# Kernel optimization log

Measured on AMD Instinct MI355X. Metric: run time of the kernel, lower is better.

The kernel has to match this reference:

```python
import jax, jax.numpy as jnp
import numpy as np

DIM = 512
HEADS = 8
HEAD_DIM = DIM // HEADS
MLP_HIDDEN = int(DIM * 4.0)
B, N = 4, 2048
LS_INIT = 1e-5
EPS = 1e-5


def _layernorm(x, w, b):
    mu = jnp.mean(x, axis=-1, keepdims=True)
    var = jnp.mean(jnp.square(x - mu), axis=-1, keepdims=True)
    return (x - mu) * jax.lax.rsqrt(var + EPS) * w + b


def setup_inputs() -> dict:
    key = jax.random.key(0)
    ks = jax.random.split(key, 12)
    s = 0.02
    return {
        "x": jax.random.normal(ks[0], (B, N, DIM), jnp.float32),
        "rel_pos_bias": jax.random.normal(ks[1], (HEADS, N, N), jnp.float32),
        "qkv_w": jax.random.normal(ks[2], (DIM, 3 * DIM), jnp.float32) * s,
        "qkv_b": jnp.zeros((3 * DIM,), jnp.float32),
        "out_w": jax.random.normal(ks[3], (DIM, DIM), jnp.float32) * s,
        "out_b": jnp.zeros((DIM,), jnp.float32),
        "ln1_w": jnp.ones((DIM,), jnp.float32),
        "ln1_b": jnp.zeros((DIM,), jnp.float32),
        "ln2_w": jnp.ones((DIM,), jnp.float32),
        "ln2_b": jnp.zeros((DIM,), jnp.float32),
        "ffn_w1": jax.random.normal(ks[4], (DIM, MLP_HIDDEN), jnp.float32) * s,
        "ffn_b1": jnp.zeros((MLP_HIDDEN,), jnp.float32),
        "ffn_w2": jax.random.normal(ks[5], (MLP_HIDDEN, DIM), jnp.float32) * s,
        "ffn_b2": jnp.zeros((DIM,), jnp.float32),
        "gamma1": jnp.full((DIM,), LS_INIT, jnp.float32),
        "gamma2": jnp.full((DIM,), LS_INIT, jnp.float32),
    }


def reference(x, rel_pos_bias, qkv_w, qkv_b, out_w, out_b, ln1_w, ln1_b,
              ln2_w, ln2_b, ffn_w1, ffn_b1, ffn_w2, ffn_b2, gamma1, gamma2):
    # Pre-norm MHA with relative-position bias
    y = _layernorm(x, ln1_w, ln1_b)                       # [B,N,C]
    qkv = y @ qkv_w + qkv_b                               # [B,N,3C]
    qkv = qkv.reshape(B, N, 3, HEADS, HEAD_DIM)
    q = jnp.transpose(qkv[:, :, 0], (0, 2, 1, 3))         # [B,H,N,D]
    k = jnp.transpose(qkv[:, :, 1], (0, 2, 1, 3))
    v = jnp.transpose(qkv[:, :, 2], (0, 2, 1, 3))
    scale = 1.0 / np.sqrt(HEAD_DIM).astype(np.float32)
    attn = jnp.einsum("bhid,bhjd->bhij", q, k) * scale    # [B,H,N,N]
    attn = attn + rel_pos_bias[None]
    attn = jax.nn.softmax(attn, axis=-1)
    out = jnp.einsum("bhij,bhjd->bhid", attn, v)          # [B,H,N,D]
    out = jnp.transpose(out, (0, 2, 1, 3)).reshape(B, N, DIM)
    out = out @ out_w + out_b
    x = x + out * gamma1                                  # layer scale, no drop-path (eval)
    # FFN with exact GELU
    y2 = _layernorm(x, ln2_w, ln2_b)
    h = jax.nn.gelu(y2 @ ffn_w1 + ffn_b1, approximate=False)
    ffn_out = h @ ffn_w2 + ffn_b2
    x = x + ffn_out * gamma2
    return x
```

## Files before the change

### kernel.cpp

```cpp
#include <hip/hip_runtime.h>
#include <hip/hip_bf16.h>
#include <math.h>

#define SEQ 2048
#define BATCH 4
#define DM 512
#define NH 8
#define HD 64
#define HID 2048
#define ROWS (BATCH * SEQ)

typedef __attribute__((ext_vector_type(8))) short short8;
typedef __attribute__((ext_vector_type(4))) float f32x4;

__device__ __forceinline__ short f2bf(float f) {
    unsigned u = __float_as_uint(f);
    u += 0x7fff + ((u >> 16) & 1);
    return (short)(u >> 16);
}

__device__ __forceinline__ void gl2lds16(const void* g, void* l) {
    __builtin_amdgcn_global_load_lds(
        (const __attribute__((address_space(1))) void*)g,
        (__attribute__((address_space(3))) void*)l, 16, 0, 0);
}

__global__ __launch_bounds__(256) void tcast_all(
    const float* __restrict__ qkv_w, const float* __restrict__ out_w,
    const float* __restrict__ w1, const float* __restrict__ w2,
    short* __restrict__ o_qkv, short* __restrict__ o_out,
    short* __restrict__ o_w1, short* __restrict__ o_w2) {
    __shared__ float tile[32][33];
    int id = blockIdx.x;
    const float* W; short* O; int K, N;
    if (id < 768)       { W = qkv_w; O = o_qkv; K = 512;  N = 1536; }
    else if (id < 1024) { W = out_w; O = o_out; K = 512;  N = 512;  id -= 768; }
    else if (id < 2048) { W = w1;    O = o_w1;  K = 512;  N = 2048; id -= 1024; }
    else                { W = w2;    O = o_w2;  K = 2048; N = 512;  id -= 2048; }
    int tn = N / 32;
    int n0 = (id % tn) * 32, k0 = (id / tn) * 32;
    int tx = threadIdx.x, ty = threadIdx.y;
#pragma unroll
    for (int i = 0; i < 4; ++i)
        tile[ty + i * 8][tx] = W[(size_t)(k0 + ty + i * 8) * N + n0 + tx];
    __syncthreads();
#pragma unroll
    for (int i = 0; i < 4; ++i)
        O[(size_t)(n0 + ty + i * 8) * K + k0 + tx] = f2bf(tile[tx][ty + i * 8]);
}

__global__ __launch_bounds__(256) void bias_prep(const float* __restrict__ bias,
                                                 short* __restrict__ biasP) {
    __shared__ float tl[4][16][68];
    int t = threadIdx.x;
    int w = t >> 6, ln = t & 63;
    int quad = ln >> 4, l15 = ln & 15;
    int tau = blockIdx.x * 4 + w;
    int jtK = tau & 31;
    int g = (tau >> 5) & 127;
    int h = tau >> 12;
    const float* src = bias + (size_t)h * SEQ * SEQ + (size_t)g * 16 * SEQ + jtK * 64;
#pragma unroll
    for (int i = 0; i < 4; ++i) {
        int row = i * 4 + quad;
        int col = l15 * 4;
        *(float4*)&tl[w][row][col] = *(const float4*)(src + (size_t)row * SEQ + col);
    }
    short* dst = biasP + (size_t)tau * 1024 + ln * 4;
#pragma unroll
    for (int ni = 0; ni < 4; ++ni) {
        float4 v = *(const float4*)&tl[w][l15][ni * 16 + quad * 4];
        float2 lo, hi;
        lo.x = v.x * 1.44269504f; lo.y = v.y * 1.44269504f;
        hi.x = v.z * 1.44269504f; hi.y = v.w * 1.44269504f;
        __hip_bfloat162 l2 = __float22bfloat162_rn(lo);
        __hip_bfloat162 h2 = __float22bfloat162_rn(hi);
        uint2 pp;
        pp.x = *(unsigned*)&l2;
        pp.y = *(unsigned*)&h2;
        *(uint2*)(dst + (size_t)ni * 256) = pp;
    }
}

__global__ __launch_bounds__(256) void ln_k(const float* __restrict__ X,
                                            const float* __restrict__ g,
                                            const float* __restrict__ bta,
                                            short* __restrict__ Y) {
    int t = threadIdx.x;
    int wv = t >> 6, ln = t & 63;
    size_t row = (size_t)blockIdx.x * 4 + wv;
    const float* xr = X + row * DM;
    float4 v0 = *(const float4*)(xr + ln * 4);
    float4 v1 = *(const float4*)(xr + 256 + ln * 4);
    float s = v0.x + v0.y + v0.z + v0.w + v1.x + v1.y + v1.z + v1.w;
    float q = v0.x * v0.x + v0.y * v0.y + v0.z * v0.z + v0.w * v0.w +
              v1.x * v1.x + v1.y * v1.y + v1.z * v1.z + v1.w * v1.w;
#pragma unroll
    for (int off = 1; off < 64; off <<= 1) {
        s += __shfl_xor(s, off);
        q += __shfl_xor(q, off);
    }
    float mean = s * (1.0f / 512.0f);
    float var = q * (1.0f / 512.0f) - mean * mean;
    float rstd = rsqrtf(var + 1e-5f);
    int c0 = ln * 4, c1 = 256 + ln * 4;
    ushort4 o0, o1;
    o0.x = (unsigned short)f2bf((v0.x - mean) * rstd * g[c0 + 0] + bta[c0 + 0]);
    o0.y = (unsigned short)f2bf((v0.y - mean) * rstd * g[c0 + 1] + bta[c0 + 1]);
    o0.z = (unsigned short)f2bf((v0.z - mean) * rstd * g[c0 + 2] + bta[c0 + 2]);
    o0.w = (unsigned short)f2bf((v0.w - mean) * rstd * g[c0 + 3] + bta[c0 + 3]);
    o1.x = (unsigned short)f2bf((v1.x - mean) * rstd * g[c1 + 0] + bta[c1 + 0]);
    o1.y = (unsigned short)f2bf((v1.y - mean) * rstd * g[c1 + 1] + bta[c1 + 1]);
    o1.z = (unsigned short)f2bf((v1.z - mean) * rstd * g[c1 + 2] + bta[c1 + 2]);
    o1.w = (unsigned short)f2bf((v1.w - mean) * rstd * g[c1 + 3] + bta[c1 + 3]);
    *(ushort4*)((unsigned short*)Y + row * DM + c0) = o0;
    *(ushort4*)((unsigned short*)Y + row * DM + c1) = o1;
}

template <int EPI, int TN>
__global__ __launch_bounds__(256) void gemm_bt(const short* __restrict__ A,
                                               const short* __restrict__ Bt,
                                               const float* __restrict__ bias,
                                               const float* __restrict__ gamma,
                                               const float* __restrict__ res,
                                               void* __restrict__ Cout,
                                               short* __restrict__ Cout2,
                                               int M, int N, int K) {
    constexpr int NI = TN / 32;
    __shared__ __attribute__((aligned(16))) short As0[128][32];
    __shared__ __attribute__((aligned(16))) short As1[128][32];
    __shared__ __attribute__((aligned(16))) short Bs0[TN][32];
    __shared__ __attribute__((aligned(16))) short Bs1[TN][32];
    int t = threadIdx.x;
    int w = t >> 6, ln = t & 63;
    int quad = ln >> 4, l15 = ln & 15;
    int n0 = blockIdx.x * TN, m0 = blockIdx.y * 128;
    int wm = (w & 1) * 64, wn = (w >> 1) * (TN / 2);

    int srow0 = w * 32 + (ln >> 2);
    int srow1 = srow0 + 16;
    int srowB = w * 16 + (ln >> 2);
    int schunk = (ln & 3) * 8;
    const short* Ag0 = A + (size_t)(m0 + srow0) * K + schunk;
    const short* Ag1 = A + (size_t)(m0 + srow1) * K + schunk;
    const short* Bg0 = Bt + (size_t)(n0 + srow0) * K + schunk;
    const short* Bg1 = Bt + (size_t)(n0 + srow1) * K + schunk;
    const short* BgB = Bt + (size_t)(n0 + srowB) * K + schunk;

    f32x4 acc[4][NI];
#pragma unroll
    for (int i = 0; i < 4; ++i)
#pragma unroll
        for (int j = 0; j < NI; ++j) acc[i][j] = (f32x4){0.f, 0.f, 0.f, 0.f};

    for (int k0 = 0; k0 < K; k0 += 64) {
        __syncthreads();
        gl2lds16(Ag0 + k0, &As0[srow0][schunk]);
        gl2lds16(Ag1 + k0, &As0[srow1][schunk]);
        gl2lds16(Ag0 + k0 + 32, &As1[srow0][schunk]);
        gl2lds16(Ag1 + k0 + 32, &As1[srow1][schunk]);
        if (TN == 128) {
            gl2lds16(Bg0 + k0, &Bs0[srow0 & (TN - 1)][schunk]);
            gl2lds16(Bg1 + k0, &Bs0[srow1 & (TN - 1)][schunk]);
            gl2lds16(Bg0 + k0 + 32, &Bs1[srow0 & (TN - 1)][schunk]);
            gl2lds16(Bg1 + k0 + 32, &Bs1[srow1 & (TN - 1)][schunk]);
        } else {
            gl2lds16(BgB + k0, &Bs0[srowB & (TN - 1)][schunk]);
            gl2lds16(BgB + k0 + 32, &Bs1[srowB & (TN - 1)][schunk]);
        }
        __syncthreads();
        {
            short8 af[4], bf[NI];
#pragma unroll
            for (int mi = 0; mi < 4; ++mi)
                af[mi] = *(const short8*)&As0[wm + mi * 16 + l15][quad * 8];
#pragma unroll
            for (int ni = 0; ni < NI; ++ni)
                bf[ni] = *(const short8*)&Bs0[wn + ni * 16 + l15][quad * 8];
#pragma unroll
            for (int mi = 0; mi < 4; ++mi)
#pragma unroll
                for (int ni = 0; ni < NI; ++ni)
                    acc[mi][ni] = __builtin_amdgcn_mfma_f32_16x16x32_bf16(
                        af[mi], bf[ni], acc[mi][ni], 0, 0, 0);
        }
        {
            short8 af[4], bf[NI];
#pragma unroll
            for (int mi = 0; mi < 4; ++mi)
                af[mi] = *(const short8*)&As1[wm + mi * 16 + l15][quad * 8];
#pragma unroll
            for (int ni = 0; ni < NI; ++ni)
                bf[ni] = *(const short8*)&Bs1[wn + ni * 16 + l15][quad * 8];
#pragma unroll
            for (int mi = 0; mi < 4; ++mi)
#pragma unroll
                for (int ni = 0; ni < NI; ++ni)
                    acc[mi][ni] = __builtin_amdgcn_mfma_f32_16x16x32_bf16(
                        af[mi], bf[ni], acc[mi][ni], 0, 0, 0);
        }
    }

    if (EPI == 3 && n0 >= 1024) {
#pragma unroll
        for (int mi = 0; mi < 4; ++mi) {
#pragma unroll
            for (int ni = 0; ni < NI; ++ni) {
                int col = n0 + wn + ni * 16 + l15;
                int d = col - 1024, hh = d >> 6, dd = d & 63;
                int row0 = m0 + wm + mi * 16 + quad * 4;
                int bb = row0 >> 11, key = row0 & 2047;
                float bs = bias[col];
                ushort4 pk;
                pk.x = (unsigned short)f2bf(acc[mi][ni][0] + bs);
                pk.y = (unsigned short)f2bf(acc[mi][ni][1] + bs);
                pk.z = (unsigned short)f2bf(acc[mi][ni][2] + bs);
                pk.w = (unsigned short)f2bf(acc[mi][ni][3] + bs);
                *(ushort4*)&Cout2[((size_t)(bb * 8 + hh) * 64 + dd) * 2048 + key] = pk;
            }
        }
    } else {
#pragma unroll
        for (int mi = 0; mi < 4; ++mi) {
#pragma unroll
            for (int ni = 0; ni < NI; ++ni) {
#pragma unroll
                for (int r = 0; r < 4; ++r) {
                    int row = m0 + wm + mi * 16 + quad * 4 + r;
                    int col = n0 + wn + ni * 16 + l15;
                    float v = acc[mi][ni][r] + bias[col];
                    if (EPI == 0) {
                        ((short*)Cout)[(size_t)row * N + col] = f2bf(v);
                    } else if (EPI == 1) {
                        float u = v * fmaf(v * v, 0.0713548162f, 1.59576912f);
                        float gg = v / (1.0f + __expf(-u));
                        ((short*)Cout)[(size_t)row * N + col] = f2bf(gg);
                    } else if (EPI == 2) {
                        ((float*)Cout)[(size_t)row * N + col] =
                            fmaf(v, gamma[col], res[(size_t)row * N + col]);
                    } else {
                        float sc = (n0 < 512) ? 0.18033688f : 1.0f;
                        ((short*)Cout)[(size_t)row * 1024 + col] = f2bf(v * sc);
                    }
                }
            }
        }
    }
}

__global__ __launch_bounds__(256, 3) void attn_k(const short* __restrict__ qkv,
                                                 const short* __restrict__ vT,
                                                 const short* __restrict__ biasP,
                                                 float* __restrict__ O0,
                                                 float* __restrict__ O1,
                                                 float* __restrict__ lp) {
    __shared__ __attribute__((aligned(16))) short Ks[2][64 * 64];
    __shared__ __attribute__((aligned(16))) short Vs[2][64 * 64];
    __shared__ __attribute__((aligned(16))) short Ps[4][2][16 * 64];
    int t = threadIdx.x;
    int w = t >> 6, ln = t & 63, quad = ln >> 4, l15 = ln & 15;
    int idx = blockIdx.x;
    int half = idx >> 9;
    int rest = idx & 511;
    int h = rest & 7, b = (rest >> 3) & 3, qt = rest >> 5;
    int qb = qt * 128 + w * 16;
    int jt0 = half * 16;
    int j0 = jt0 * 64;
    const size_t cbase = (size_t)b * SEQ * 1024;

    const short* qrow0 = qkv + cbase + (size_t)(qb + l15) * 1024 + h * 64;
    const short* qrow1 = qrow0 + (size_t)64 * 1024;
    short8 qf[2][2];
    qf[0][0] = *(const short8*)(qrow0 + quad * 8);
    qf[0][1] = *(const short8*)(qrow0 + 32 + quad * 8);
    qf[1][0] = *(const short8*)(qrow1 + quad * 8);
    qf[1][1] = *(const short8*)(qrow1 + 32 + quad * 8);

    int kr = t >> 3, kc = t & 7;
    int sc = (kc ^ (kr & 7)) * 8;
    const short* kgS = qkv + cbase + 512 + h * 64 + sc;
    const short* vgS = vT + (size_t)(b * 8 + h) * 64 * 2048 + sc;

    int g0 = qt * 8 + w;
    const short* bp0 = biasP + ((size_t)(h * 128 + g0) * 32) * 1024 + ln * 4;
    const short* bp1 = biasP + ((size_t)(h * 128 + g0 + 4) * 32) * 1024 + ln * 4;

    short8 ones;
#pragma unroll
    for (int i = 0; i < 8; ++i) ones[i] = (short)0x3F80;

    f32x4 o[2][4], ol[2];
#pragma unroll
    for (int qg = 0; qg < 2; ++qg) {
#pragma unroll
        for (int db = 0; db < 4; ++db) o[qg][db] = (f32x4){0.f, 0.f, 0.f, 0.f};
        ol[qg] = (f32x4){0.f, 0.f, 0.f, 0.f};
    }

    int sw7 = l15 & 7;

    gl2lds16(kgS + (size_t)(j0 + kr) * 1024,      &Ks[0][t * 8]);
    gl2lds16(kgS + (size_t)(j0 + 32 + kr) * 1024, &Ks[0][2048 + t * 8]);
    gl2lds16(vgS + (size_t)kr * 2048 + j0,        &Vs[0][t * 8]);
    gl2lds16(vgS + (size_t)(32 + kr) * 2048 + j0, &Vs[0][2048 + t * 8]);
    uint2 bbc[2][4];
#pragma unroll
    for (int ni = 0; ni < 4; ++ni) {
        bbc[0][ni] = *(const uint2*)(bp0 + (size_t)jt0 * 1024 + ni * 256);
        bbc[1][ni] = *(const uint2*)(bp1 + (size_t)jt0 * 1024 + ni * 256);
    }

    int cur = 0;
    for (int jt = jt0; jt < jt0 + 16; ++jt) {
        __syncthreads();
        int jn = (jt < jt0 + 15) ? (jt + 1) : jt;
        int j1 = jn * 64;
        int nxt = cur ^ 1;
        gl2lds16(kgS + (size_t)(j1 + kr) * 1024,      &Ks[nxt][t * 8]);
        gl2lds16(kgS + (size_t)(j1 + 32 + kr) * 1024, &Ks[nxt][2048 + t * 8]);
        gl2lds16(vgS + (size_t)kr * 2048 + j1,        &Vs[nxt][t * 8]);
        gl2lds16(vgS + (size_t)(32 + kr) * 2048 + j1, &Vs[nxt][2048 + t * 8]);

        f32x4 s4[2][4];
#pragma unroll
        for (int ni = 0; ni < 4; ++ni) {
            short8 k0 = *(const short8*)&Ks[cur][(ni * 16 + l15) * 64 + ((quad ^ sw7) * 8)];
            short8 k1 = *(const short8*)&Ks[cur][(ni * 16 + l15) * 64 + (((4 + quad) ^ sw7) * 8)];
#pragma unroll
            for (int qg = 0; qg < 2; ++qg) {
                uint2 bb = bbc[qg][ni];
                f32x4 z;
                z[0] = __uint_as_float(bb.x << 16);
                z[1] = __uint_as_float(bb.x & 0xffff0000u);
                z[2] = __uint_as_float(bb.y << 16);
                z[3] = __uint_as_float(bb.y & 0xffff0000u);
                bbc[qg][ni] = *(const uint2*)((qg ? bp1 : bp0) + (size_t)jn * 1024 + ni * 256);
                z = __builtin_amdgcn_mfma_f32_16x16x32_bf16(k0, qf[qg][0], z, 0, 0, 0);
                s4[qg][ni] = __builtin_amdgcn_mfma_f32_16x16x32_bf16(k1, qf[qg][1], z, 0, 0, 0);
            }
        }
#pragma unroll
        for (int qg = 0; qg < 2; ++qg) {
#pragma unroll
            for (int ni = 0; ni < 4; ++ni) {
                float2 plo, phi;
                plo.x = exp2f(s4[qg][ni][0]);
                plo.y = exp2f(s4[qg][ni][1]);
                phi.x = exp2f(s4[qg][ni][2]);
                phi.y = exp2f(s4[qg][ni][3]);
                __hip_bfloat162 l2 = __float22bfloat162_rn(plo);
                __hip_bfloat162 h2 = __float22bfloat162_rn(phi);
                union { uint2 u; } pp;
                pp.u.x = *(unsigned*)&l2;
                pp.u.y = *(unsigned*)&h2;
                int c = ni * 2 + (quad >> 1);
                *(uint2*)&Ps[w][qg][l15 * 64 + ((c ^ sw7) * 8) + (quad & 1) * 4] = pp.u;
            }
        }
#pragma unroll
        for (int kk = 0; kk < 2; ++kk) {
            short8 ap0 = *(const short8*)&Ps[w][0][l15 * 64 + (((kk * 4 + quad) ^ sw7) * 8)];
            short8 ap1 = *(const short8*)&Ps[w][1][l15 * 64 + (((kk * 4 + quad) ^ sw7) * 8)];
#pragma unroll
            for (int db = 0; db < 4; ++db) {
                short8 vv = *(const short8*)&Vs[cur][(db * 16 + l15) * 64 + (((kk * 4 + quad) ^ sw7) * 8)];
                o[0][db] = __builtin_amdgcn_mfma_f32_16x16x32_bf16(ap0, vv, o[0][db], 0, 0, 0);
                o[1][db] = __builtin_amdgcn_mfma_f32_16x16x32_bf16(ap1, vv, o[1][db], 0, 0, 0);
            }
            ol[0] = __builtin_amdgcn_mfma_f32_16x16x32_bf16(ap0, ones, ol[0], 0, 0, 0);
            ol[1] = __builtin_amdgcn_mfma_f32_16x16x32_bf16(ap1, ones, ol[1], 0, 0, 0);
        }
        cur = nxt;
    }
    float* Od = half ? O1 : O0;
    float* ld = lp + half * (32 * 2048);
#pragma unroll
    for (int qg = 0; qg < 2; ++qg) {
#pragma unroll
        for (int r = 0; r < 4; ++r) {
            int qloc = qb + qg * 64 + quad * 4 + r;
            int qrow_g = b * SEQ + qloc;
#pragma unroll
            for (int db = 0; db < 4; ++db) {
                Od[(size_t)qrow_g * DM + h * 64 + db * 16 + l15] = o[qg][db][r];
            }
            if (l15 == 0)
                ld[(size_t)(b * 8 + h) * 2048 + qloc] = ol[qg][r];
        }
    }
}

__global__ __launch_bounds__(256) void comb_k(const float* __restrict__ O0,
                                              const float* __restrict__ O1,
                                              const float* __restrict__ lp,
                                              short* __restrict__ Aout) {
    int t = threadIdx.x;
    int wv = t >> 6, ln = t & 63;
    size_t row = (size_t)blockIdx.x * 4 + wv;
    int b = (int)(row >> 11), q = (int)(row & 2047);
    int h = ln >> 3;
    float la = lp[(size_t)(b * 8 + h) * 2048 + q];
    float lb = lp[32 * 2048 + (size_t)(b * 8 + h) * 2048 + q];
    float inv = 1.0f / (la + lb);
    const float* p0 = O0 + row * DM + ln * 8;
    const float* p1 = O1 + row * DM + ln * 8;
    float4 a0 = *(const float4*)p0;
    float4 a1 = *(const float4*)(p0 + 4);
    float4 c0 = *(const float4*)p1;
    float4 c1 = *(const float4*)(p1 + 4);
    short8 o;
    o[0] = f2bf((a0.x + c0.x) * inv);
    o[1] = f2bf((a0.y + c0.y) * inv);
    o[2] = f2bf((a0.z + c0.z) * inv);
    o[3] = f2bf((a0.w + c0.w) * inv);
    o[4] = f2bf((a1.x + c1.x) * inv);
    o[5] = f2bf((a1.y + c1.y) * inv);
    o[6] = f2bf((a1.z + c1.z) * inv);
    o[7] = f2bf((a1.w + c1.w) * inv);
    *(short8*)(Aout + row * DM + ln * 8) = o;
}

extern "C" void kernel_launch(void* const* d_in, const int* in_sizes, int n_in,
                              void* d_out, int out_size, void* d_ws, size_t ws_size,
                              hipStream_t stream) {
    const float* x      = (const float*)d_in[0];
    const float* bias   = (const float*)d_in[1];
    const float* qkv_w  = (const float*)d_in[2];
    const float* qkv_b  = (const float*)d_in[3];
    const float* out_w  = (const float*)d_in[4];
    const float* out_b  = (const float*)d_in[5];
    const float* ln1_w  = (const float*)d_in[6];
    const float* ln1_b  = (const float*)d_in[7];
    const float* ln2_w  = (const float*)d_in[8];
    const float* ln2_b  = (const float*)d_in[9];
    const float* ffn_w1 = (const float*)d_in[10];
    const float* ffn_b1 = (const float*)d_in[11];
    const float* ffn_w2 = (const float*)d_in[12];
    const float* ffn_b2 = (const float*)d_in[13];
    const float* gamma1 = (const float*)d_in[14];
    const float* gamma2 = (const float*)d_in[15];
    float* out = (float*)d_out;

    short* wqkvT = (short*)d_ws;
    short* woutT = wqkvT + (size_t)1536 * 512;
    short* w1T   = woutT + (size_t)512 * 512;
    short* w2T   = w1T + (size_t)2048 * 512;
    short* y1    = w2T + (size_t)512 * 2048;
    short* qkvB  = y1 + (size_t)ROWS * DM;
    short* vTb   = qkvB + (size_t)ROWS * 1024;
    short* aoutB = vTb + (size_t)32 * 64 * 2048;
    float* x1    = (float*)(aoutB + (size_t)ROWS * DM);
    float* opart1 = x1 + (size_t)ROWS * DM;
    float* lpart  = opart1 + (size_t)ROWS * DM;
    short* biasPw = (short*)(lpart + 2 * 32 * 2048);
    float* opart0 = x1;
    short* hB    = qkvB;

    tcast_all<<<3072, dim3(32, 8), 0, stream>>>(qkv_w, out_w, ffn_w1, ffn_w2,
                                                wqkvT, woutT, w1T, w2T);
    bias_prep<<<8192, 256, 0, stream>>>(bias, biasPw);
    ln_k<<<ROWS / 4, 256, 0, stream>>>(x, ln1_w, ln1_b, y1);
    gemm_bt<3, 128><<<dim3(1536 / 128, ROWS / 128), 256, 0, stream>>>(
        y1, wqkvT, qkv_b, nullptr, nullptr, qkvB, vTb, ROWS, 1536, 512);
    attn_k<<<1024, 256, 0, stream>>>(qkvB, vTb, biasPw, opart0, opart1, lpart);
    comb_k<<<ROWS / 4, 256, 0, stream>>>(opart0, opart1, lpart, aoutB);
    gemm_bt<2, 64><<<dim3(512 / 64, ROWS / 128), 256, 0, stream>>>(
        aoutB, woutT, out_b, gamma1, x, x1, nullptr, ROWS, 512, 512);
    ln_k<<<ROWS / 4, 256, 0, stream>>>(x1, ln2_w, ln2_b, y1);
    gemm_bt<1, 128><<<dim3(2048 / 128, ROWS / 128), 256, 0, stream>>>(
        y1, w1T, ffn_b1, nullptr, nullptr, hB, nullptr, ROWS, 2048, 512);
    gemm_bt<2, 64><<<dim3(512 / 64, ROWS / 128), 256, 0, stream>>>(
        hB, w2T, ffn_b2, gamma2, x1, out, nullptr, ROWS, 512, 2048);
}
```

Before: 463.9 us.

## Drop split-K attention and combine kernel; restructure bias prep for coalesced reads

Attention no longer splits the key dimension into two halves. Each block now loops over all 32 key tiles and normalizes and writes bf16 output directly, which removes the fp32 partial-output buffers and the separate combine kernel. The bias preprocessing kernel now reads full 1024-wide row segments per block, converts them into a wider LDS tile, then scatters them into the tiled layout, using fewer and larger blocks. The cost is half as many attention blocks (512), which lowers parallelism and latency hiding on a GPU with many CUs.

After: 453.4 us. -2.3%, faster.

```diff
diff --git a/kernel.cpp b/kernel.cpp
--- a/kernel.cpp
+++ b/kernel.cpp
@@ -51,25 +51,17 @@
 
 __global__ __launch_bounds__(256) void bias_prep(const float* __restrict__ bias,
                                                  short* __restrict__ biasP) {
-    __shared__ float tl[4][16][68];
+    __shared__ short tl[16][1032];
     int t = threadIdx.x;
-    int w = t >> 6, ln = t & 63;
-    int quad = ln >> 4, l15 = ln & 15;
-    int tau = blockIdx.x * 4 + w;
-    int jtK = tau & 31;
-    int g = (tau >> 5) & 127;
-    int h = tau >> 12;
-    const float* src = bias + (size_t)h * SEQ * SEQ + (size_t)g * 16 * SEQ + jtK * 64;
-#pragma unroll
-    for (int i = 0; i < 4; ++i) {
-        int row = i * 4 + quad;
-        int col = l15 * 4;
-        *(float4*)&tl[w][row][col] = *(const float4*)(src + (size_t)row * SEQ + col);
-    }
-    short* dst = biasP + (size_t)tau * 1024 + ln * 4;
-#pragma unroll
-    for (int ni = 0; ni < 4; ++ni) {
-        float4 v = *(const float4*)&tl[w][l15][ni * 16 + quad * 4];
+    int w = t >> 6, ln = t & 63, quad = ln >> 4, l15 = ln & 15;
+    int id = blockIdx.x;
+    int half = id & 1;
+    int g = (id >> 1) & 127;
+    int h = id >> 8;
+    const float* src = bias + (size_t)h * SEQ * SEQ + (size_t)g * 16 * SEQ + half * 1024;
+#pragma unroll
+    for (int i = 0; i < 16; ++i) {
+        float4 v = *(const float4*)(src + (size_t)i * SEQ + t * 4);
         float2 lo, hi;
         lo.x = v.x * 1.44269504f; lo.y = v.y * 1.44269504f;
         hi.x = v.z * 1.44269504f; hi.y = v.w * 1.44269504f;
@@ -78,7 +70,19 @@
         uint2 pp;
         pp.x = *(unsigned*)&l2;
         pp.y = *(unsigned*)&h2;
-        *(uint2*)(dst + (size_t)ni * 256) = pp;
+        *(uint2*)&tl[i][t * 4] = pp;
+    }
+    __syncthreads();
+    int jtbase = half * 16;
+#pragma unroll
+    for (int u = 0; u < 4; ++u) {
+        int jl = w * 4 + u;
+        int tau = (h * 128 + g) * 32 + jtbase + jl;
+#pragma unroll
+        for (int ni = 0; ni < 4; ++ni) {
+            uint2 pp = *(const uint2*)&tl[l15][jl * 64 + ni * 16 + quad * 4];
+            *(uint2*)(biasP + (size_t)tau * 1024 + ni * 256 + ln * 4) = pp;
+        }
     }
 }
 
@@ -251,21 +255,15 @@
 __global__ __launch_bounds__(256, 3) void attn_k(const short* __restrict__ qkv,
                                                  const short* __restrict__ vT,
                                                  const short* __restrict__ biasP,
-                                                 float* __restrict__ O0,
-                                                 float* __restrict__ O1,
-                                                 float* __restrict__ lp) {
+                                                 short* __restrict__ Aout) {
     __shared__ __attribute__((aligned(16))) short Ks[2][64 * 64];
     __shared__ __attribute__((aligned(16))) short Vs[2][64 * 64];
     __shared__ __attribute__((aligned(16))) short Ps[4][2][16 * 64];
     int t = threadIdx.x;
     int w = t >> 6, ln = t & 63, quad = ln >> 4, l15 = ln & 15;
     int idx = blockIdx.x;
-    int half = idx >> 9;
-    int rest = idx & 511;
-    int h = rest & 7, b = (rest >> 3) & 3, qt = rest >> 5;
+    int h = idx & 7, b = (idx >> 3) & 3, qt = idx >> 5;
     int qb = qt * 128 + w * 16;
-    int jt0 = half * 16;
-    int j0 = jt0 * 64;
     const size_t cbase = (size_t)b * SEQ * 1024;
 
     const short* qrow0 = qkv + cbase + (size_t)(qb + l15) * 1024 + h * 64;
@@ -299,21 +297,21 @@
 
     int sw7 = l15 & 7;
 
-    gl2lds16(kgS + (size_t)(j0 + kr) * 1024,      &Ks[0][t * 8]);
-    gl2lds16(kgS + (size_t)(j0 + 32 + kr) * 1024, &Ks[0][2048 + t * 8]);
-    gl2lds16(vgS + (size_t)kr * 2048 + j0,        &Vs[0][t * 8]);
-    gl2lds16(vgS + (size_t)(32 + kr) * 2048 + j0, &Vs[0][2048 + t * 8]);
+    gl2lds16(kgS,                              &Ks[0][t * 8]);
+    gl2lds16(kgS + (size_t)32 * 1024,          &Ks[0][2048 + t * 8]);
+    gl2lds16(vgS,                              &Vs[0][t * 8]);
+    gl2lds16(vgS + (size_t)32 * 2048,          &Vs[0][2048 + t * 8]);
     uint2 bbc[2][4];
 #pragma unroll
     for (int ni = 0; ni < 4; ++ni) {
-        bbc[0][ni] = *(const uint2*)(bp0 + (size_t)jt0 * 1024 + ni * 256);
-        bbc[1][ni] = *(const uint2*)(bp1 + (size_t)jt0 * 1024 + ni * 256);
+        bbc[0][ni] = *(const uint2*)(bp0 + ni * 256);
+        bbc[1][ni] = *(const uint2*)(bp1 + ni * 256);
     }
 
     int cur = 0;
-    for (int jt = jt0; jt < jt0 + 16; ++jt) {
+    for (int jt = 0; jt < 32; ++jt) {
         __syncthreads();
-        int jn = (jt < jt0 + 15) ? (jt + 1) : jt;
+        int jn = (jt < 31) ? (jt + 1) : jt;
         int j1 = jn * 64;
         int nxt = cur ^ 1;
         gl2lds16(kgS + (size_t)(j1 + kr) * 1024,      &Ks[nxt][t * 8]);
@@ -372,52 +370,19 @@
         }
         cur = nxt;
     }
-    float* Od = half ? O1 : O0;
-    float* ld = lp + half * (32 * 2048);
 #pragma unroll
     for (int qg = 0; qg < 2; ++qg) {
 #pragma unroll
         for (int r = 0; r < 4; ++r) {
-            int qloc = qb + qg * 64 + quad * 4 + r;
-            int qrow_g = b * SEQ + qloc;
+            float inv = 1.0f / ol[qg][r];
+            int qrow_g = b * SEQ + qb + qg * 64 + quad * 4 + r;
 #pragma unroll
             for (int db = 0; db < 4; ++db) {
-                Od[(size_t)qrow_g * DM + h * 64 + db * 16 + l15] = o[qg][db][r];
-            }
-            if (l15 == 0)
-                ld[(size_t)(b * 8 + h) * 2048 + qloc] = ol[qg][r];
-        }
-    }
-}
-
-__global__ __launch_bounds__(256) void comb_k(const float* __restrict__ O0,
-                                              const float* __restrict__ O1,
-                                              const float* __restrict__ lp,
-                                              short* __restrict__ Aout) {
-    int t = threadIdx.x;
-    int wv = t >> 6, ln = t & 63;
-    size_t row = (size_t)blockIdx.x * 4 + wv;
-    int b = (int)(row >> 11), q = (int)(row & 2047);
-    int h = ln >> 3;
-    float la = lp[(size_t)(b * 8 + h) * 2048 + q];
-    float lb = lp[32 * 2048 + (size_t)(b * 8 + h) * 2048 + q];
-    float inv = 1.0f / (la + lb);
-    const float* p0 = O0 + row * DM + ln * 8;
-    const float* p1 = O1 + row * DM + ln * 8;
-    float4 a0 = *(const float4*)p0;
-    float4 a1 = *(const float4*)(p0 + 4);
-    float4 c0 = *(const float4*)p1;
-    float4 c1 = *(const float4*)(p1 + 4);
-    short8 o;
-    o[0] = f2bf((a0.x + c0.x) * inv);
-    o[1] = f2bf((a0.y + c0.y) * inv);
-    o[2] = f2bf((a0.z + c0.z) * inv);
-    o[3] = f2bf((a0.w + c0.w) * inv);
-    o[4] = f2bf((a1.x + c1.x) * inv);
-    o[5] = f2bf((a1.y + c1.y) * inv);
-    o[6] = f2bf((a1.z + c1.z) * inv);
-    o[7] = f2bf((a1.w + c1.w) * inv);
-    *(short8*)(Aout + row * DM + ln * 8) = o;
+                Aout[(size_t)qrow_g * DM + h * 64 + db * 16 + l15] =
+                    f2bf(o[qg][db][r] * inv);
+            }
+        }
+    }
 }
 
 extern "C" void kernel_launch(void* const* d_in, const int* in_sizes, int n_in,
@@ -450,20 +415,16 @@
     short* vTb   = qkvB + (size_t)ROWS * 1024;
     short* aoutB = vTb + (size_t)32 * 64 * 2048;
     float* x1    = (float*)(aoutB + (size_t)ROWS * DM);
-    float* opart1 = x1 + (size_t)ROWS * DM;
-    float* lpart  = opart1 + (size_t)ROWS * DM;
-    short* biasPw = (short*)(lpart + 2 * 32 * 2048);
-    float* opart0 = x1;
+    short* biasPw = (short*)(x1 + (size_t)ROWS * DM);
     short* hB    = qkvB;
 
     tcast_all<<<3072, dim3(32, 8), 0, stream>>>(qkv_w, out_w, ffn_w1, ffn_w2,
                                                 wqkvT, woutT, w1T, w2T);
-    bias_prep<<<8192, 256, 0, stream>>>(bias, biasPw);
+    bias_prep<<<2048, 256, 0, stream>>>(bias, biasPw);
     ln_k<<<ROWS / 4, 256, 0, stream>>>(x, ln1_w, ln1_b, y1);
     gemm_bt<3, 128><<<dim3(1536 / 128, ROWS / 128), 256, 0, stream>>>(
         y1, wqkvT, qkv_b, nullptr, nullptr, qkvB, vTb, ROWS, 1536, 512);
-    attn_k<<<1024, 256, 0, stream>>>(qkvB, vTb, biasPw, opart0, opart1, lpart);
-    comb_k<<<ROWS / 4, 256, 0, stream>>>(opart0, opart1, lpart, aoutB);
+    attn_k<<<512, 256, 0, stream>>>(qkvB, vTb, biasPw, aoutB);
     gemm_bt<2, 64><<<dim3(512 / 64, ROWS / 128), 256, 0, stream>>>(
         aoutB, woutT, out_b, gamma1, x, x1, nullptr, ROWS, 512, 512);
     ln_k<<<ROWS / 4, 256, 0, stream>>>(x1, ln2_w, ln2_b, y1);
```
